# Performance work log

Measured on AMD Instinct MI355X. Metric: run time of the kernel, lower is better.

Reference implementation:

```python
import jax, jax.numpy as jnp
import numpy as np

G = 8          # num_groups
GIN = 2048 // G   # group_in_features
GOUT = 2048 // G  # group_out_features


def setup_inputs() -> dict:
    key = jax.random.key(0)
    kx, kw, kb = jax.random.split(key, 3)
    x = jax.random.normal(kx, (8192, 2048), dtype=jnp.float32)
    # per-group linear params, torch nn.Linear default init scale ~ U(-1/sqrt(fan_in), ...)
    bound = 1.0 / np.sqrt(GIN)
    W = jax.random.uniform(kw, (G, GIN, GOUT), minval=-bound, maxval=bound, dtype=jnp.float32)
    b = jax.random.uniform(kb, (G, GOUT), minval=-bound, maxval=bound, dtype=jnp.float32)
    # rational activation coeffs, init p=[1,0,0,0], q=[1,0,0] per group
    p = jnp.tile(jnp.array([1.0, 0.0, 0.0, 0.0], dtype=jnp.float32), (G, 1))
    q = jnp.tile(jnp.array([1.0, 0.0, 0.0], dtype=jnp.float32), (G, 1))
    return {"x": x, "W": W, "b": b, "p": p, "q": q}


def _rational(y, p, q):
    # y: [N, G, GOUT]; p: [G, 4]; q: [G, 3] -> broadcast over N and GOUT
    p = p[None, :, :, None]  # [1,G,4,1]
    q = q[None, :, :, None]  # [1,G,3,1]
    y2 = y * y
    y3 = y2 * y
    num = p[:, :, 0] + p[:, :, 1] * y + p[:, :, 2] * y2 + p[:, :, 3] * y3
    den = 1.0 + jnp.abs(q[:, :, 0] * y + q[:, :, 1] * y2 + q[:, :, 2] * y3)
    return num / den


def reference(x, W, b, p, q):
    N = x.shape[0]
    xg = x.reshape(N, G, GIN)                       # chunk along last dim
    y = jnp.einsum('ngi,gio->ngo', xg, W) + b[None]  # grouped GEMM, [N,G,GOUT]
    out = _rational(y, p, q)
    return out.reshape(N, G * GOUT)                 # cat along last dim
```

## Files before the change

kernel.cpp:

```cpp
#include <hip/hip_runtime.h>
#include <hip/hip_bf16.h>

#define G_ 8
#define GIN_ 256
#define GOUT_ 256
#define NROWS_ 8192
#define LDX_ 2048

typedef __attribute__((ext_vector_type(4))) float f32x4;
typedef __attribute__((ext_vector_type(8))) short bf16x8;

__device__ __forceinline__ void lds_barrier() {
    asm volatile("s_waitcnt lgkmcnt(0)\n\ts_barrier" ::: "memory");
}

__global__ __launch_bounds__(256) void wprep_kernel(const float* __restrict__ W,
                                                    __hip_bfloat16* __restrict__ Wt) {
    __shared__ float tile[64][65];
    const int bid = blockIdx.x;
    const int g  = bid >> 4;
    const int ot = (bid >> 2) & 3;
    const int it = bid & 3;
    const float* Wg = W + g * GIN_ * GOUT_;
    __hip_bfloat16* Wtg = Wt + g * GIN_ * GOUT_;
    const int lane_o = threadIdx.x & 63;
    const int sub    = threadIdx.x >> 6;
#pragma unroll
    for (int r = 0; r < 16; ++r) {
        int i = r * 4 + sub;
        tile[i][lane_o] = Wg[(it * 64 + i) * GOUT_ + ot * 64 + lane_o];
    }
    __syncthreads();
#pragma unroll
    for (int r = 0; r < 16; ++r) {
        int o = r * 4 + sub;
        Wtg[(ot * 64 + o) * GIN_ + it * 64 + lane_o] = __float2bfloat16(tile[lane_o][o]);
    }
}

__global__ __launch_bounds__(512, 4) void gkan_kernel(const float* __restrict__ x,
                                                      const __hip_bfloat16* __restrict__ Wt,
                                                      const float* __restrict__ bias,
                                                      const float* __restrict__ pc,
                                                      const float* __restrict__ qc,
                                                      float* __restrict__ out) {
    __shared__ __align__(16) __hip_bfloat16 As[2][32 * 256];

    const int bid    = blockIdx.x;
    const int g      = bid & 7;
    const int mblock = bid >> 3;
    const int row0   = mblock * 128;

    const int t    = threadIdx.x;
    const int wave = t >> 6;
    const int lane = t & 63;
    const int lm   = lane & 15;
    const int quad = lane >> 4;

    bf16x8 Breg[2][8];
    {
        const __hip_bfloat16* Wg = Wt + (size_t)g * (GIN_ * GOUT_)
                                      + (size_t)(wave * 32) * GIN_;
#pragma unroll
        for (int nt = 0; nt < 2; ++nt)
#pragma unroll
            for (int c = 0; c < 8; ++c)
                Breg[nt][c] = *(const bf16x8*)(Wg + (size_t)(nt * 16 + lm) * GIN_
                                                  + c * 32 + quad * 8);
    }

    const float p0 = pc[g * 4 + 0], p1 = pc[g * 4 + 1];
    const float p2 = pc[g * 4 + 2], p3 = pc[g * 4 + 3];
    const float q0 = qc[g * 3 + 0], q1 = qc[g * 3 + 1], q2 = qc[g * 3 + 2];
    float bb[2];
#pragma unroll
    for (int nt = 0; nt < 2; ++nt)
        bb[nt] = bias[g * GOUT_ + wave * 32 + nt * 16 + lm];

    const int sr = t >> 4;
    const int su = t & 15;
    const float* xs = x + (size_t)(row0 + sr) * LDX_ + g * GIN_ + su * 16;
    const int go0 = (((2 * su)     ^ (sr & 7)) * 8);
    const int go1 = (((2 * su + 1) ^ (sr & 7)) * 8);
    __hip_bfloat16* row_b0 = &As[0][sr * 256];
    __hip_bfloat16* row_b1 = &As[1][sr * 256];

    f32x4 st0, st1, st2, st3;
    st0 = *(const f32x4*)(xs);
    st1 = *(const f32x4*)(xs + 4);
    st2 = *(const f32x4*)(xs + 8);
    st3 = *(const f32x4*)(xs + 12);
    {
        union { __hip_bfloat16 h[8]; bf16x8 v; } ca, cb;
        ca.h[0] = __float2bfloat16(st0.x); ca.h[1] = __float2bfloat16(st0.y);
        ca.h[2] = __float2bfloat16(st0.z); ca.h[3] = __float2bfloat16(st0.w);
        ca.h[4] = __float2bfloat16(st1.x); ca.h[5] = __float2bfloat16(st1.y);
        ca.h[6] = __float2bfloat16(st1.z); ca.h[7] = __float2bfloat16(st1.w);
        cb.h[0] = __float2bfloat16(st2.x); cb.h[1] = __float2bfloat16(st2.y);
        cb.h[2] = __float2bfloat16(st2.z); cb.h[3] = __float2bfloat16(st2.w);
        cb.h[4] = __float2bfloat16(st3.x); cb.h[5] = __float2bfloat16(st3.y);
        cb.h[6] = __float2bfloat16(st3.z); cb.h[7] = __float2bfloat16(st3.w);
        *(bf16x8*)(row_b0 + go0) = ca.v;
        *(bf16x8*)(row_b0 + go1) = cb.v;
    }
    lds_barrier();

#pragma unroll 1
    for (int s = 0; s < 4; ++s) {
        if (s < 3) {
            const float* xn = xs + (size_t)(s + 1) * 32 * LDX_;
            st0 = *(const f32x4*)(xn);
            st1 = *(const f32x4*)(xn + 4);
            st2 = *(const f32x4*)(xn + 8);
            st3 = *(const f32x4*)(xn + 12);
        }

        const __hip_bfloat16* slab = As[s & 1];
        f32x4 acc[2][2] = {};
#pragma unroll
        for (int c = 0; c < 8; ++c) {
            bf16x8 af[2];
#pragma unroll
            for (int mt = 0; mt < 2; ++mt) {
                const int gh = (c * 4 + quad) ^ (lm & 7);
                af[mt] = *(const bf16x8*)(slab + (mt * 16 + lm) * 256 + gh * 8);
            }
#pragma unroll
            for (int mt = 0; mt < 2; ++mt)
#pragma unroll
                for (int nt = 0; nt < 2; ++nt)
                    acc[mt][nt] = __builtin_amdgcn_mfma_f32_16x16x32_bf16(
                        af[mt], Breg[nt][c], acc[mt][nt], 0, 0, 0);
        }

#pragma unroll
        for (int nt = 0; nt < 2; ++nt) {
            const int col = g * GOUT_ + wave * 32 + nt * 16 + lm;
#pragma unroll
            for (int mt = 0; mt < 2; ++mt)
#pragma unroll
                for (int r = 0; r < 4; ++r) {
                    const int row = row0 + s * 32 + mt * 16 + quad * 4 + r;
                    const float y   = acc[mt][nt][r] + bb[nt];
                    const float num = p0 + y * (p1 + y * (p2 + y * p3));
                    const float den = 1.0f + fabsf(y * (q0 + y * (q1 + y * q2)));
                    out[(size_t)row * LDX_ + col] = num * __builtin_amdgcn_rcpf(den);
                }
        }

        if (s < 3) {
            __hip_bfloat16* dst = (s & 1) ? row_b0 : row_b1;
            union { __hip_bfloat16 h[8]; bf16x8 v; } ca, cb;
            ca.h[0] = __float2bfloat16(st0.x); ca.h[1] = __float2bfloat16(st0.y);
            ca.h[2] = __float2bfloat16(st0.z); ca.h[3] = __float2bfloat16(st0.w);
            ca.h[4] = __float2bfloat16(st1.x); ca.h[5] = __float2bfloat16(st1.y);
            ca.h[6] = __float2bfloat16(st1.z); ca.h[7] = __float2bfloat16(st1.w);
            cb.h[0] = __float2bfloat16(st2.x); cb.h[1] = __float2bfloat16(st2.y);
            cb.h[2] = __float2bfloat16(st2.z); cb.h[3] = __float2bfloat16(st2.w);
            cb.h[4] = __float2bfloat16(st3.x); cb.h[5] = __float2bfloat16(st3.y);
            cb.h[6] = __float2bfloat16(st3.z); cb.h[7] = __float2bfloat16(st3.w);
            *(bf16x8*)(dst + go0) = ca.v;
            *(bf16x8*)(dst + go1) = cb.v;
            lds_barrier();
        }
    }
}

extern "C" void kernel_launch(void* const* d_in, const int* in_sizes, int n_in,
                              void* d_out, int out_size, void* d_ws, size_t ws_size,
                              hipStream_t stream) {
    const float* x = (const float*)d_in[0];
    const float* W = (const float*)d_in[1];
    const float* b = (const float*)d_in[2];
    const float* p = (const float*)d_in[3];
    const float* q = (const float*)d_in[4];
    float* out = (float*)d_out;

    __hip_bfloat16* Wt = (__hip_bfloat16*)d_ws;

    wprep_kernel<<<128, 256, 0, stream>>>(W, Wt);
    gkan_kernel<<<512, 512, 0, stream>>>(x, Wt, b, p, q, out);
}
```

Baseline: 136.6 us.

## Split grouped GEMM into many small single-slab blocks with half-column tiles

```diff
diff --git a/kernel.cpp b/kernel.cpp
--- a/kernel.cpp
+++ b/kernel.cpp
@@ -38,29 +38,39 @@
     }
 }
 
-__global__ __launch_bounds__(512, 4) void gkan_kernel(const float* __restrict__ x,
+__global__ __launch_bounds__(256, 4) void gkan_kernel(const float* __restrict__ x,
                                                       const __hip_bfloat16* __restrict__ Wt,
                                                       const float* __restrict__ bias,
                                                       const float* __restrict__ pc,
                                                       const float* __restrict__ qc,
                                                       float* __restrict__ out) {
-    __shared__ __align__(16) __hip_bfloat16 As[2][32 * 256];
+    __shared__ __align__(16) __hip_bfloat16 As[32 * 256];
 
     const int bid    = blockIdx.x;
     const int g      = bid & 7;
-    const int mblock = bid >> 3;
-    const int row0   = mblock * 128;
+    const int ch     = (bid >> 3) & 1;
+    const int mblock = bid >> 4;
+    const int row0   = mblock * 32;
 
     const int t    = threadIdx.x;
     const int wave = t >> 6;
     const int lane = t & 63;
     const int lm   = lane & 15;
     const int quad = lane >> 4;
+    const int colbase = ch * 128 + wave * 32;
+
+    const int sr = t >> 3;
+    const int su = t & 7;
+    const float* xs = x + (size_t)(row0 + sr) * LDX_ + g * GIN_ + su * 32;
+    f32x4 st[8];
+#pragma unroll
+    for (int j = 0; j < 8; ++j)
+        st[j] = *(const f32x4*)(xs + j * 4);
 
     bf16x8 Breg[2][8];
     {
         const __hip_bfloat16* Wg = Wt + (size_t)g * (GIN_ * GOUT_)
-                                      + (size_t)(wave * 32) * GIN_;
+                                      + (size_t)colbase * GIN_;
 #pragma unroll
         for (int nt = 0; nt < 2; ++nt)
 #pragma unroll
@@ -75,94 +85,53 @@
     float bb[2];
 #pragma unroll
     for (int nt = 0; nt < 2; ++nt)
-        bb[nt] = bias[g * GOUT_ + wave * 32 + nt * 16 + lm];
+        bb[nt] = bias[g * GOUT_ + colbase + nt * 16 + lm];
 
-    const int sr = t >> 4;
-    const int su = t & 15;
-    const float* xs = x + (size_t)(row0 + sr) * LDX_ + g * GIN_ + su * 16;
-    const int go0 = (((2 * su)     ^ (sr & 7)) * 8);
-    const int go1 = (((2 * su + 1) ^ (sr & 7)) * 8);
-    __hip_bfloat16* row_b0 = &As[0][sr * 256];
-    __hip_bfloat16* row_b1 = &As[1][sr * 256];
-
-    f32x4 st0, st1, st2, st3;
-    st0 = *(const f32x4*)(xs);
-    st1 = *(const f32x4*)(xs + 4);
-    st2 = *(const f32x4*)(xs + 8);
-    st3 = *(const f32x4*)(xs + 12);
     {
-        union { __hip_bfloat16 h[8]; bf16x8 v; } ca, cb;
-        ca.h[0] = __float2bfloat16(st0.x); ca.h[1] = __float2bfloat16(st0.y);
-        ca.h[2] = __float2bfloat16(st0.z); ca.h[3] = __float2bfloat16(st0.w);
-        ca.h[4] = __float2bfloat16(st1.x); ca.h[5] = __float2bfloat16(st1.y);
-        ca.h[6] = __float2bfloat16(st1.z); ca.h[7] = __float2bfloat16(st1.w);
-        cb.h[0] = __float2bfloat16(st2.x); cb.h[1] = __float2bfloat16(st2.y);
-        cb.h[2] = __float2bfloat16(st2.z); cb.h[3] = __float2bfloat16(st2.w);
-        cb.h[4] = __float2bfloat16(st3.x); cb.h[5] = __float2bfloat16(st3.y);
-        cb.h[6] = __float2bfloat16(st3.z); cb.h[7] = __float2bfloat16(st3.w);
-        *(bf16x8*)(row_b0 + go0) = ca.v;
-        *(bf16x8*)(row_b0 + go1) = cb.v;
+        __hip_bfloat16* rowp = &As[sr * 256];
+#pragma unroll
+        for (int k = 0; k < 4; ++k) {
+            union { __hip_bfloat16 h[8]; bf16x8 v; } cv;
+            const f32x4 a = st[2 * k], b = st[2 * k + 1];
+            cv.h[0] = __float2bfloat16(a.x); cv.h[1] = __float2bfloat16(a.y);
+            cv.h[2] = __float2bfloat16(a.z); cv.h[3] = __float2bfloat16(a.w);
+            cv.h[4] = __float2bfloat16(b.x); cv.h[5] = __float2bfloat16(b.y);
+            cv.h[6] = __float2bfloat16(b.z); cv.h[7] = __float2bfloat16(b.w);
+            *(bf16x8*)(rowp + (((4 * su + k) ^ (sr & 7)) * 8)) = cv.v;
+        }
     }
     lds_barrier();
 
-#pragma unroll 1
-    for (int s = 0; s < 4; ++s) {
-        if (s < 3) {
-            const float* xn = xs + (size_t)(s + 1) * 32 * LDX_;
-            st0 = *(const f32x4*)(xn);
-            st1 = *(const f32x4*)(xn + 4);
-            st2 = *(const f32x4*)(xn + 8);
-            st3 = *(const f32x4*)(xn + 12);
+    f32x4 acc[2][2] = {};
+#pragma unroll
+    for (int c = 0; c < 8; ++c) {
+        bf16x8 af[2];
+#pragma unroll
+        for (int mt = 0; mt < 2; ++mt) {
+            const int gh = (c * 4 + quad) ^ (lm & 7);
+            af[mt] = *(const bf16x8*)(As + (mt * 16 + lm) * 256 + gh * 8);
         }
-
-        const __hip_bfloat16* slab = As[s & 1];
-        f32x4 acc[2][2] = {};
 #pragma unroll
-        for (int c = 0; c < 8; ++c) {
-            bf16x8 af[2];
+        for (int mt = 0; mt < 2; ++mt)
 #pragma unroll
-            for (int mt = 0; mt < 2; ++mt) {
-                const int gh = (c * 4 + quad) ^ (lm & 7);
-                af[mt] = *(const bf16x8*)(slab + (mt * 16 + lm) * 256 + gh * 8);
-            }
-#pragma unroll
-            for (int mt = 0; mt < 2; ++mt)
-#pragma unroll
-                for (int nt = 0; nt < 2; ++nt)
-                    acc[mt][nt] = __builtin_amdgcn_mfma_f32_16x16x32_bf16(
-                        af[mt], Breg[nt][c], acc[mt][nt], 0, 0, 0);
-        }
+            for (int nt = 0; nt < 2; ++nt)
+                acc[mt][nt] = __builtin_amdgcn_mfma_f32_16x16x32_bf16(
+                    af[mt], Breg[nt][c], acc[mt][nt], 0, 0, 0);
+    }
 
 #pragma unroll
-        for (int nt = 0; nt < 2; ++nt) {
-            const int col = g * GOUT_ + wave * 32 + nt * 16 + lm;
+    for (int nt = 0; nt < 2; ++nt) {
+        const int col = g * GOUT_ + colbase + nt * 16 + lm;
 #pragma unroll
-            for (int mt = 0; mt < 2; ++mt)
+        for (int mt = 0; mt < 2; ++mt)
 #pragma unroll
-                for (int r = 0; r < 4; ++r) {
-                    const int row = row0 + s * 32 + mt * 16 + quad * 4 + r;
-                    const float y   = acc[mt][nt][r] + bb[nt];
-                    const float num = p0 + y * (p1 + y * (p2 + y * p3));
-                    const float den = 1.0f + fabsf(y * (q0 + y * (q1 + y * q2)));
-                    out[(size_t)row * LDX_ + col] = num * __builtin_amdgcn_rcpf(den);
-                }
-        }
-
-        if (s < 3) {
-            __hip_bfloat16* dst = (s & 1) ? row_b0 : row_b1;
-            union { __hip_bfloat16 h[8]; bf16x8 v; } ca, cb;
-            ca.h[0] = __float2bfloat16(st0.x); ca.h[1] = __float2bfloat16(st0.y);
-            ca.h[2] = __float2bfloat16(st0.z); ca.h[3] = __float2bfloat16(st0.w);
-            ca.h[4] = __float2bfloat16(st1.x); ca.h[5] = __float2bfloat16(st1.y);
-            ca.h[6] = __float2bfloat16(st1.z); ca.h[7] = __float2bfloat16(st1.w);
-            cb.h[0] = __float2bfloat16(st2.x); cb.h[1] = __float2bfloat16(st2.y);
-            cb.h[2] = __float2bfloat16(st2.z); cb.h[3] = __float2bfloat16(st2.w);
-            cb.h[4] = __float2bfloat16(st3.x); cb.h[5] = __float2bfloat16(st3.y);
-            cb.h[6] = __float2bfloat16(st3.z); cb.h[7] = __float2bfloat16(st3.w);
-            *(bf16x8*)(dst + go0) = ca.v;
-            *(bf16x8*)(dst + go1) = cb.v;
-            lds_barrier();
-        }
+            for (int r = 0; r < 4; ++r) {
+                const int row = row0 + mt * 16 + quad * 4 + r;
+                const float y   = acc[mt][nt][r] + bb[nt];
+                const float num = p0 + y * (p1 + y * (p2 + y * p3));
+                const float den = 1.0f + fabsf(y * (q0 + y * (q1 + y * q2)));
+                out[(size_t)row * LDX_ + col] = num * __builtin_amdgcn_rcpf(den);
+            }
     }
 }
 
@@ -179,5 +148,5 @@
     __hip_bfloat16* Wt = (__hip_bfloat16*)d_ws;
 
     wprep_kernel<<<128, 256, 0, stream>>>(W, Wt);
-    gkan_kernel<<<512, 512, 0, stream>>>(x, Wt, b, p, q, out);
+    gkan_kernel<<<4096, 256, 0, stream>>>(x, Wt, b, p, q, out);
 }
```

Measured after the change: 150.8 us. +10.4%, slower.
